# Kernel optimization log

Hardware: AMD Instinct MI355X
Metric: run time of the kernel (lower is better)

The kernel has to match this reference:

```python
import jax, jax.numpy as jnp
import numpy as np

H = 2048   # hidden_size
E = 4096   # intermediate_size
N = 16     # ssm_state_size
K = 4      # conv_kernel
R = 128    # time_step_rank
B_SZ = 2
L = 2048


def setup_inputs() -> dict:
    key = jax.random.key(0)
    ks = jax.random.split(key, 9)
    s = lambda fan: 1.0 / np.sqrt(fan)
    hidden_states = jax.random.normal(ks[0], (B_SZ, L, H), dtype=jnp.float32)
    in_proj_w = jax.random.normal(ks[1], (2 * E, H), dtype=jnp.float32) * s(H)
    conv_w = jax.random.normal(ks[2], (E, 1, K), dtype=jnp.float32) * s(K)
    conv_b = jax.random.normal(ks[3], (E,), dtype=jnp.float32) * 0.01
    x_proj_w = jax.random.normal(ks[4], (R + 2 * N, E), dtype=jnp.float32) * s(E)
    dt_proj_w = jax.random.normal(ks[5], (E, R), dtype=jnp.float32) * s(R)
    dt_proj_b = jax.random.normal(ks[6], (E,), dtype=jnp.float32) * 0.01
    A_log = jnp.log(jnp.broadcast_to(jnp.arange(1, N + 1, dtype=jnp.float32)[None, :], (E, N)))
    D = jnp.ones((E,), dtype=jnp.float32)
    out_proj_w = jax.random.normal(ks[7], (H, E), dtype=jnp.float32) * s(E)
    return {
        "hidden_states": hidden_states,
        "in_proj_w": in_proj_w,
        "conv_w": conv_w,
        "conv_b": conv_b,
        "x_proj_w": x_proj_w,
        "dt_proj_w": dt_proj_w,
        "dt_proj_b": dt_proj_b,
        "A_log": A_log,
        "D": D,
        "out_proj_w": out_proj_w,
    }


def _mamba_fwd(hidden_states, in_proj_w, conv_w, conv_b, x_proj_w,
               dt_proj_w, dt_proj_b, A_log, D, out_proj_w):
    # in_proj -> [B, L, 2E] -> transpose -> [B, 2E, L] -> chunk
    proj = jnp.einsum('blh,eh->ble', hidden_states, in_proj_w)
    proj = jnp.transpose(proj, (0, 2, 1))              # [B, 2E, L]
    u, gate = jnp.split(proj, 2, axis=1)               # each [B, E, L]

    # causal depthwise conv1d (pad K-1 left), then silu
    x = jax.lax.conv_general_dilated(
        u, conv_w, window_strides=(1,), padding=[(K - 1, 0)],
        dimension_numbers=('NCH', 'OIH', 'NCH'), feature_group_count=E)
    x = jax.nn.silu(x + conv_b[None, :, None])          # [B, E, L]

    # x_proj -> dt, B, C
    x_bl = jnp.transpose(x, (0, 2, 1))                  # [B, L, E]
    x_dbl = jnp.einsum('ble,re->blr', x_bl, x_proj_w)   # [B, L, R+2N]
    dt_low, Bmat, Cmat = jnp.split(x_dbl, [R, R + N], axis=-1)
    dt = jax.nn.softplus(jnp.einsum('blr,er->ble', dt_low, dt_proj_w) + dt_proj_b)  # [B, L, E]

    A = -jnp.exp(A_log)                                 # [E, N]

    # selective scan over time; carry state [B, E, N]
    def step(s, inp):
        dt_t, u_t, B_t, C_t = inp                       # [B,E],[B,E],[B,N],[B,N]
        dA = jnp.exp(dt_t[..., None] * A[None])         # [B, E, N]
        s = s * dA + (dt_t * u_t)[..., None] * B_t[:, None, :]
        y_t = jnp.einsum('ben,bn->be', s, C_t)
        return s, y_t

    xs = (jnp.transpose(dt, (1, 0, 2)),                 # [L, B, E]
          jnp.transpose(x, (2, 0, 1)),                  # [L, B, E]
          jnp.transpose(Bmat, (1, 0, 2)),               # [L, B, N]
          jnp.transpose(Cmat, (1, 0, 2)))               # [L, B, N]
    s0 = jnp.zeros((hidden_states.shape[0], E, N), dtype=jnp.float32)
    _, ys = jax.lax.scan(step, s0, xs)                  # ys: [L, B, E]

    y = jnp.transpose(ys, (1, 2, 0))                    # [B, E, L]
    y = y + x * D[None, :, None]
    y = y * jax.nn.silu(gate)
    out = jnp.einsum('bel,he->blh', y, out_proj_w)      # [B, L, H]
    return out


def reference(hidden_states, in_proj_w, conv_w, conv_b, x_proj_w,
              dt_proj_w, dt_proj_b, A_log, D, out_proj_w):
    return _mamba_fwd(hidden_states, in_proj_w, conv_w, conv_b, x_proj_w,
                      dt_proj_w, dt_proj_b, A_log, D, out_proj_w)
```

## Files before the change

kernel.cpp:

```cpp
#include <hip/hip_runtime.h>
#include <math.h>

#define Hd 2048
#define Ed 4096
#define Nssm 16
#define Rrank 128
#define Bb 2
#define Ll 2048
#define Mrows (Bb*Ll)
#define XDBL_C 160
#define Cc 64
#define Tc (Ll/Cc)

typedef unsigned short u16;
typedef short bf16x8 __attribute__((ext_vector_type(8)));
typedef float f32x4 __attribute__((ext_vector_type(4)));
typedef u16 us4 __attribute__((ext_vector_type(4)));
typedef u16 us8 __attribute__((ext_vector_type(8)));

__device__ __forceinline__ u16 f2bf(float f) {
    unsigned u = __float_as_uint(f);
    u += 0x7FFFu + ((u >> 16) & 1u);
    return (u16)(u >> 16);
}
__device__ __forceinline__ float bf2f(u16 h) {
    return __uint_as_float((unsigned)h << 16);
}
__device__ __forceinline__ float fexp(float x)  { return __expf(x); }
__device__ __forceinline__ float fsig(float x)  { return __builtin_amdgcn_rcpf(1.f + __expf(-x)); }
__device__ __forceinline__ float fsoftplus(float z) {
    return fmaxf(z, 0.f) + __logf(1.f + __expf(-fabsf(z)));
}

__device__ __forceinline__ void stage_tile(const char* g, int ldbytes, char* lds, int tid)
{
#pragma unroll
    for (int q = 0; q < 4; ++q) {
        int idx = q * 256 + tid;
        int row = idx >> 3;
        int cb  = (idx & 7) << 4;
        int sb  = cb ^ ((row & 7) << 4);
        __builtin_amdgcn_global_load_lds(
            (const __attribute__((address_space(1))) void*)(g + (size_t)row * ldbytes + sb),
            (__attribute__((address_space(3))) void*)(lds + (size_t)idx * 16),
            16, 0, 0);
    }
}

__device__ __forceinline__ void stage_half(const char* g, int ldbytes, char* lds, int tid)
{
#pragma unroll
    for (int q = 0; q < 2; ++q) {
        int idx = q * 512 + tid;
        int row = idx >> 3;
        int cb  = (idx & 7) << 4;
        int sb  = cb ^ ((row & 7) << 4);
        __builtin_amdgcn_global_load_lds(
            (const __attribute__((address_space(1))) void*)(g + (size_t)row * ldbytes + sb),
            (__attribute__((address_space(3))) void*)(lds + (size_t)idx * 16),
            16, 0, 0);
    }
}

#define NK8  32
#define NKP8 16

__global__ __launch_bounds__(512, 2)
void gemm_8ph_inproj(const u16* __restrict__ A, const u16* __restrict__ Bw,
                     u16* __restrict__ C)
{
    __shared__ __align__(16) char lds[131072];
    const int tid = threadIdx.x;
    const int bm = blockIdx.y * 256;
    const int bn = blockIdx.x * 256;
    const int lane = tid & 63;
    const int wv = tid >> 6;
    const int wm = wv >> 2;
    const int wn = wv & 3;
    const int lr = lane & 15, kg = lane >> 4;

    f32x4 acc[8][4];
#pragma unroll
    for (int m = 0; m < 8; ++m)
#pragma unroll
        for (int n = 0; n < 4; ++n) acc[m][n] = (f32x4){0.f, 0.f, 0.f, 0.f};

    bf16x8 av[8], bv[4];

#define ASLOT(d, h) (lds + ((d)*2 + (h)) * 16384)
#define BSLOT(d, h) (lds + 65536 + ((d)*2 + (h)) * 16384)

#define STAGE_AH(t, h) stage_half((const char*)A  + ((size_t)(bm + (h)*128) * Hd + (t)*64) * 2, Hd*2, ASLOT((t)&1, h), tid)
#define STAGE_BH(t, h) stage_half((const char*)Bw + ((size_t)(bn + (h)*128) * Hd + (t)*64) * 2, Hd*2, BSLOT((t)&1, h), tid)

#define READ_ASUB(d, s) { \
    const char* slot_ = ASLOT(d, wm); \
    _Pragma("unroll") for (int f = 0; f < 4; ++f) { \
        int row = (s)*64 + f*16 + lr; int sw = (row & 7) << 4; \
        const char* rb = slot_ + row * 128; \
        av[f*2+0] = *(const bf16x8*)(rb + ((kg*16) ^ sw)); \
        av[f*2+1] = *(const bf16x8*)(rb + ((64 + kg*16) ^ sw)); } }
#define READ_BSUB(d, u) { \
    const char* slot_ = BSLOT(d, (wn >> 1)); \
    _Pragma("unroll") for (int f = 0; f < 2; ++f) { \
        int row = (wn & 1)*64 + (u)*32 + f*16 + lr; int sw = (row & 7) << 4; \
        const char* rb = slot_ + row * 128; \
        bv[f*2+0] = *(const bf16x8*)(rb + ((kg*16) ^ sw)); \
        bv[f*2+1] = *(const bf16x8*)(rb + ((64 + kg*16) ^ sw)); } }
#define QUAD(s, u) { \
    _Pragma("unroll") for (int f = 0; f < 4; ++f) \
    _Pragma("unroll") for (int g2 = 0; g2 < 2; ++g2) { \
        acc[(s)*4+f][(u)*2+g2] = __builtin_amdgcn_mfma_f32_16x16x32_bf16(av[f*2+0], bv[g2*2+0], acc[(s)*4+f][(u)*2+g2], 0, 0, 0); \
        acc[(s)*4+f][(u)*2+g2] = __builtin_amdgcn_mfma_f32_16x16x32_bf16(av[f*2+1], bv[g2*2+1], acc[(s)*4+f][(u)*2+g2], 0, 0, 0); } }

#define BAR __builtin_amdgcn_s_barrier()
#define PRIO_MFMA(s, u) BAR; __builtin_amdgcn_s_setprio(1); QUAD(s, u); __builtin_amdgcn_s_setprio(0)
#define VMW(n) { asm volatile("s_waitcnt vmcnt(" #n ")" ::: "memory"); __builtin_amdgcn_sched_barrier(0); }

    STAGE_BH(0, 0); STAGE_BH(0, 1); STAGE_AH(0, 0); STAGE_AH(0, 1);
    STAGE_BH(1, 0);
    VMW(2);
    BAR;

    for (int i = 0; i < NKP8; ++i) {
        const int o = 2*i + 1, t2 = 2*i + 2, t3 = 2*i + 3;
        READ_ASUB(0, 0); READ_BSUB(0, 0);
        STAGE_BH(o, 1);
        PRIO_MFMA(0, 0); BAR;
        READ_ASUB(0, 1);
        STAGE_AH(o, 0);
        PRIO_MFMA(1, 0); BAR;
        READ_BSUB(0, 1);
        STAGE_AH(o, 1);
        PRIO_MFMA(1, 1); BAR;
        READ_ASUB(0, 0);
        if (t2 < NK8) STAGE_BH(t2, 0);
        PRIO_MFMA(0, 1);
        if (i == NKP8 - 1) { VMW(0); } else { VMW(2); }
        BAR;
        READ_ASUB(1, 0); READ_BSUB(1, 0);
        if (t2 < NK8) STAGE_BH(t2, 1);
        PRIO_MFMA(0, 0); BAR;
        READ_ASUB(1, 1);
        if (t2 < NK8) STAGE_AH(t2, 0);
        PRIO_MFMA(1, 0); BAR;
        READ_BSUB(1, 1);
        if (t2 < NK8) STAGE_AH(t2, 1);
        PRIO_MFMA(1, 1); BAR;
        READ_ASUB(1, 0);
        if (t3 < NK8) STAGE_BH(t3, 0);
        PRIO_MFMA(0, 1);
        VMW(2);
        BAR;
    }

#pragma unroll
    for (int m = 0; m < 8; ++m) {
        int rbase = bm + wm * 128 + m * 16 + kg * 4;
#pragma unroll
        for (int n = 0; n < 4; ++n) {
            int col = bn + wn * 64 + n * 16 + lr;
#pragma unroll
            for (int r = 0; r < 4; ++r)
                C[(size_t)(rbase + r) * (2 * Ed) + col] = f2bf(acc[m][n][r]);
        }
    }
#undef ASLOT
#undef BSLOT
#undef STAGE_AH
#undef STAGE_BH
#undef READ_ASUB
#undef READ_BSUB
#undef QUAD
#undef BAR
#undef PRIO_MFMA
#undef VMW
}

template<int EPI, int CBF16>
__global__ __launch_bounds__(256)
void gemm_bf16(const u16* __restrict__ A, const u16* __restrict__ Bw,
               void* __restrict__ Cp, const float* __restrict__ bias,
               int Nv, int Ksub, int lda, int ldb, int ldc, size_t zstride)
{
    __shared__ __align__(16) char lds[32768];
    char* ldsA = lds;
    char* ldsB = lds + 16384;
    const int tid = threadIdx.x;
    const int bm = blockIdx.y * 128;
    const int bn = blockIdx.x * 128;
    const int lane = tid & 63, wv = tid >> 6;
    const int wr = (wv >> 1) * 64, wc = (wv & 1) * 64;
    const int lr = lane & 15, kg = lane >> 4;
    const int kbeg = blockIdx.z * Ksub;

    f32x4 acc[4][4];
#pragma unroll
    for (int m = 0; m < 4; ++m)
#pragma unroll
        for (int n = 0; n < 4; ++n) acc[m][n] = (f32x4){0.f, 0.f, 0.f, 0.f};

    for (int k0 = kbeg; k0 < kbeg + Ksub; k0 += 64) {
        stage_tile((const char*)A  + ((size_t)bm * lda + k0) * 2, lda * 2, ldsA, tid);
        stage_tile((const char*)Bw + ((size_t)bn * ldb + k0) * 2, ldb * 2, ldsB, tid);
        __syncthreads();
#pragma unroll
        for (int kk = 0; kk < 2; ++kk) {
            const int bc = kk * 64 + kg * 16;
            bf16x8 bfr[4], af[4];
#pragma unroll
            for (int n = 0; n < 4; ++n) {
                int row = wc + n * 16 + lr;
                bfr[n] = *(const bf16x8*)(ldsB + row * 128 + (bc ^ ((row & 7) << 4)));
            }
#pragma unroll
            for (int m = 0; m < 4; ++m) {
                int row = wr + m * 16 + lr;
                af[m] = *(const bf16x8*)(ldsA + row * 128 + (bc ^ ((row & 7) << 4)));
            }
#pragma unroll
            for (int m = 0; m < 4; ++m)
#pragma unroll
                for (int n = 0; n < 4; ++n)
                    acc[m][n] = __builtin_amdgcn_mfma_f32_16x16x32_bf16(af[m], bfr[n], acc[m][n], 0, 0, 0);
        }
        __syncthreads();
    }

    if (zstride) Cp = (void*)((float*)Cp + (size_t)blockIdx.z * zstride);

#pragma unroll
    for (int m = 0; m < 4; ++m) {
        int rbase = bm + wr + m * 16 + kg * 4;
#pragma unroll
        for (int n = 0; n < 4; ++n) {
            int col = bn + wc + n * 16 + lr;
            if (col < Nv) {
#pragma unroll
                for (int r = 0; r < 4; ++r) {
                    float v = acc[m][n][r];
                    if (EPI == 1) v = fsoftplus(v + bias[col]);
                    if (CBF16) ((u16*)Cp)[(size_t)(rbase + r) * ldc + col] = f2bf(v);
                    else       ((float*)Cp)[(size_t)(rbase + r) * ldc + col] = v;
                }
            }
        }
    }
}

__global__ __launch_bounds__(256)
void reduce_cast(const float* __restrict__ part, float* __restrict__ outf,
                 u16* __restrict__ outb, int cnt, size_t stride, int total)
{
    int i = blockIdx.x * 256 + threadIdx.x;
    if (i < total) {
        float v = 0.f;
        for (int z = 0; z < cnt; z++) v += part[(size_t)z * stride + i];
        outf[i] = v;
        outb[i] = f2bf(v);
    }
}

__global__ __launch_bounds__(256)
void cast_w(const float* __restrict__ s, u16* __restrict__ d, int n)
{
    int i = (blockIdx.x * 256 + threadIdx.x) * 8;
    if (i >= n) return;
    float4 a = *(const float4*)(s + i);
    float4 b = *(const float4*)(s + i + 4);
    us8 o;
    o[0] = f2bf(a.x); o[1] = f2bf(a.y); o[2] = f2bf(a.z); o[3] = f2bf(a.w);
    o[4] = f2bf(b.x); o[5] = f2bf(b.y); o[6] = f2bf(b.z); o[7] = f2bf(b.w);
    *(us8*)(d + i) = o;
}

__global__ __launch_bounds__(256)
void cast_wx(const float* __restrict__ s, u16* __restrict__ d)
{
    int i4 = (blockIdx.x * 256 + threadIdx.x) * 4;
    int row = i4 >> 12;
    us4 o = (us4){0, 0, 0, 0};
    if (row < XDBL_C) {
        float4 v = *(const float4*)(s + i4);
        o[0] = f2bf(v.x); o[1] = f2bf(v.y); o[2] = f2bf(v.z); o[3] = f2bf(v.w);
    }
    *(us4*)(d + i4) = o;
}

__global__ __launch_bounds__(256)
void conv_silu_bf(const u16* __restrict__ proj, const float* __restrict__ cw,
                  const float* __restrict__ cb, u16* __restrict__ x)
{
    const int e  = blockIdx.x * 256 + threadIdx.x;
    const int t0 = blockIdx.y * 32;
    const int bz = blockIdx.z;
    const float4 w4 = *(const float4*)(cw + (size_t)e * 4);
    const float bias = cb[e];
    const size_t base = (size_t)bz * Ll * (2 * Ed) + e;

    float u0 = 0.f, u1 = 0.f, u2 = 0.f;
    if (t0 >= 3) {
        u0 = bf2f(proj[base + (size_t)(t0 - 3) * (2 * Ed)]);
        u1 = bf2f(proj[base + (size_t)(t0 - 2) * (2 * Ed)]);
        u2 = bf2f(proj[base + (size_t)(t0 - 1) * (2 * Ed)]);
    }
    size_t xo = ((size_t)(bz * Ll + t0)) * Ed + e;
#pragma unroll 4
    for (int t = t0; t < t0 + 32; ++t) {
        float u3 = bf2f(proj[base + (size_t)t * (2 * Ed)]);
        float acc = bias;
        acc = fmaf(w4.x, u0, acc);
        acc = fmaf(w4.y, u1, acc);
        acc = fmaf(w4.z, u2, acc);
        acc = fmaf(w4.w, u3, acc);
        float sx = acc * fsig(acc);
        x[xo] = f2bf(sx);
        xo += Ed;
        u0 = u1; u1 = u2; u2 = u3;
    }
}

__global__ __launch_bounds__(256)
void scan_part1(const u16* __restrict__ proj, const u16* __restrict__ x,
                const float* __restrict__ xdbl, const float* __restrict__ Alog,
                float* __restrict__ S, float* __restrict__ sumdt)
{
    const int e = blockIdx.x * 256 + threadIdx.x;
    const int c = blockIdx.y;
    const int b = blockIdx.z;

    float Ae[Nssm];
#pragma unroll
    for (int n = 0; n < Nssm; n++) Ae[n] = -fexp(Alog[(size_t)e * Nssm + n]);

    float s[Nssm];
#pragma unroll
    for (int n = 0; n < Nssm; n++) s[n] = 0.f;
    float sdt = 0.f;

    const size_t row0 = (size_t)b * Ll + (size_t)c * Tc;
    for (int t = 0; t < Tc; ++t) {
        size_t r = row0 + t;
        float dtv = bf2f(proj[r * (2 * Ed) + e]);
        float uv  = bf2f(x[r * Ed + e]);
        const float* p = xdbl + r * XDBL_C + Rrank;
        float du = dtv * uv;
        sdt += dtv;
#pragma unroll
        for (int n = 0; n < Nssm; n++)
            s[n] = fmaf(s[n], fexp(dtv * Ae[n]), du * p[n]);
    }

    float* sp = S + ((((size_t)b * Cc + c) * Ed + e) * Nssm);
#pragma unroll
    for (int n = 0; n < Nssm; n += 4)
        *(float4*)(sp + n) = make_float4(s[n], s[n+1], s[n+2], s[n+3]);
    sumdt[((size_t)b * Cc + c) * Ed + e] = sdt;
}

__global__ __launch_bounds__(256)
void scan_mid(float* __restrict__ S, const float* __restrict__ sumdt,
              const float* __restrict__ Alog)
{
    const int idx = blockIdx.x * 256 + threadIdx.x;
    const int n = idx & (Nssm - 1);
    const int e = (idx >> 4) & (Ed - 1);
    const int b = idx >> 16;
    const float Ae = -fexp(Alog[(size_t)e * Nssm + n]);
    float carry = 0.f;
    for (int c = 0; c < Cc; ++c) {
        size_t off = (((size_t)b * Cc + c) * Ed + e) * Nssm + n;
        float sl = S[off];
        float P  = fexp(Ae * sumdt[((size_t)b * Cc + c) * Ed + e]);
        S[off] = carry;
        carry = fmaf(P, carry, sl);
    }
}

__global__ __launch_bounds__(256)
void scan_part2(const u16* __restrict__ proj, u16* __restrict__ x,
                const float* __restrict__ xdbl, const float* __restrict__ Alog,
                const float* __restrict__ Dvec, const float* __restrict__ S)
{
    const int e = blockIdx.x * 256 + threadIdx.x;
    const int c = blockIdx.y;
    const int b = blockIdx.z;

    float Ae[Nssm];
#pragma unroll
    for (int n = 0; n < Nssm; n++) Ae[n] = -fexp(Alog[(size_t)e * Nssm + n]);
    const float Dv = Dvec[e];

    float s[Nssm];
    const float* sp = S + ((((size_t)b * Cc + c) * Ed + e) * Nssm);
#pragma unroll
    for (int n = 0; n < Nssm; n += 4) {
        float4 v = *(const float4*)(sp + n);
        s[n] = v.x; s[n+1] = v.y; s[n+2] = v.z; s[n+3] = v.w;
    }

    const size_t row0 = (size_t)b * Ll + (size_t)c * Tc;
    for (int t = 0; t < Tc; ++t) {
        size_t r = row0 + t;
        float dtv = bf2f(proj[r * (2 * Ed) + e]);
        float uv  = bf2f(x[r * Ed + e]);
        float gv  = bf2f(proj[r * (2 * Ed) + Ed + e]);
        const float* p = xdbl + r * XDBL_C + Rrank;
        float du = dtv * uv;
        float y = 0.f;
#pragma unroll
        for (int n = 0; n < Nssm; n++) {
            float dA = fexp(dtv * Ae[n]);
            s[n] = fmaf(s[n], dA, du * p[n]);
            y = fmaf(s[n], p[Nssm + n], y);
        }
        float yv = (y + uv * Dv) * (gv * fsig(gv));
        x[r * Ed + e] = f2bf(yv);
    }
}

extern "C" void kernel_launch(void* const* d_in, const int* in_sizes, int n_in,
                              void* d_out, int out_size, void* d_ws, size_t ws_size,
                              hipStream_t stream) {
    const float* hs    = (const float*)d_in[0];
    const float* w_in  = (const float*)d_in[1];
    const float* cw    = (const float*)d_in[2];
    const float* cb    = (const float*)d_in[3];
    const float* w_x   = (const float*)d_in[4];
    const float* w_dt  = (const float*)d_in[5];
    const float* b_dt  = (const float*)d_in[6];
    const float* Alog  = (const float*)d_in[7];
    const float* Dvec  = (const float*)d_in[8];
    const float* w_out = (const float*)d_in[9];
    float* out = (float*)d_out;

    char* w = (char*)d_ws;
    u16*  proj_bf  = (u16*)w;
    u16*  x_bf     = (u16*)(w + 67108864);
    u16*  w_in_bf  = (u16*)(w + 100663296);
    u16*  w_out_bf = (u16*)(w + 134217728);
    u16*  hs_bf    = (u16*)(w + 150994944);
    u16*  w_x_bf   = (u16*)(w + 167772160);
    u16*  w_dt_bf  = (u16*)(w + 169869312);
    float* xdbl    = (float*)(w + 170917888);
    u16*  xdbl_bf  = (u16*)(w + 173539328);
    float* part    = (float*)(w + 174850048);
    float* sumdt   = (float*)(w + 185335808);
    float* S       = (float*)(w + 187432960);

    dim3 blk(256);

    cast_w<<<dim3(8192), blk, 0, stream>>>(w_in, w_in_bf, 2 * Ed * Hd);
    cast_w<<<dim3(4096), blk, 0, stream>>>(w_out, w_out_bf, Hd * Ed);
    cast_w<<<dim3(256),  blk, 0, stream>>>(w_dt, w_dt_bf, Ed * Rrank);
    cast_wx<<<dim3(1024), blk, 0, stream>>>(w_x, w_x_bf);
    cast_w<<<dim3(4096), blk, 0, stream>>>(hs, hs_bf, Mrows * Hd);

    gemm_8ph_inproj<<<dim3(2 * Ed / 256, Mrows / 256), dim3(512), 0, stream>>>(
        hs_bf, w_in_bf, proj_bf);

    conv_silu_bf<<<dim3(Ed / 256, Ll / 32, Bb), blk, 0, stream>>>(proj_bf, cw, cb, x_bf);

    gemm_bf16<0, 0><<<dim3(2, 32, 4), blk, 0, stream>>>(
        x_bf, w_x_bf, part, nullptr, XDBL_C, Ed / 4, Ed, Ed, XDBL_C,
        (size_t)Mrows * XDBL_C);
    reduce_cast<<<dim3((Mrows * XDBL_C + 255) / 256), blk, 0, stream>>>(
        part, xdbl, xdbl_bf, 4, (size_t)Mrows * XDBL_C, Mrows * XDBL_C);

    gemm_bf16<1, 1><<<dim3(32, 32, 1), blk, 0, stream>>>(
        xdbl_bf, w_dt_bf, proj_bf, b_dt, Ed, Rrank, XDBL_C, Rrank, 2 * Ed, 0);

    scan_part1<<<dim3(Ed / 256, Cc, Bb), blk, 0, stream>>>(
        proj_bf, x_bf, xdbl, Alog, S, sumdt);
    scan_mid<<<dim3(Bb * Ed * Nssm / 256), blk, 0, stream>>>(S, sumdt, Alog);
    scan_part2<<<dim3(Ed / 256, Cc, Bb), blk, 0, stream>>>(
        proj_bf, x_bf, xdbl, Alog, Dvec, S);

    gemm_bf16<0, 0><<<dim3(16, 32, 1), blk, 0, stream>>>(
        x_bf, w_out_bf, out, nullptr, Hd, Ed, Ed, Ed, Hd, 0);
}
```

Baseline: 437.4 us.

## Replace in/out projection GEMMs with shared triple-buffered 256x128 kernel

Introduces a templated triple-buffered LDS GEMM with a 256x128 tile and uses it for both the in_proj and out_proj GEMMs. It replaces the double-buffered 256x256 in_proj kernel and the generic 128x128 gemm for out_proj. The deeper prefetch is meant to hide global load latency and the smaller N tile to increase block count. The 144KB LDS footprint likely limits residency to one block per CU, and smaller tiles reduce operand reuse.

```diff
diff --git a/kernel.cpp b/kernel.cpp
--- a/kernel.cpp
+++ b/kernel.cpp
@@ -62,118 +62,97 @@
     }
 }
 
-#define NK8  32
-#define NKP8 16
-
+template<int NKT, int CBF16>
 __global__ __launch_bounds__(512, 2)
-void gemm_8ph_inproj(const u16* __restrict__ A, const u16* __restrict__ Bw,
-                     u16* __restrict__ C)
-{
-    __shared__ __align__(16) char lds[131072];
+void gemm_3buf(const u16* __restrict__ A, const u16* __restrict__ Bw,
+               void* __restrict__ Cp, int ld, int ldc)
+{
+    __shared__ __align__(16) char lds[147456];
     const int tid = threadIdx.x;
     const int bm = blockIdx.y * 256;
-    const int bn = blockIdx.x * 256;
+    const int bn = blockIdx.x * 128;
     const int lane = tid & 63;
     const int wv = tid >> 6;
-    const int wm = wv >> 2;
-    const int wn = wv & 3;
+    const int wm = wv >> 1;
+    const int wn = wv & 1;
     const int lr = lane & 15, kg = lane >> 4;
 
-    f32x4 acc[8][4];
-#pragma unroll
-    for (int m = 0; m < 8; ++m)
-#pragma unroll
-        for (int n = 0; n < 4; ++n) acc[m][n] = (f32x4){0.f, 0.f, 0.f, 0.f};
-
-    bf16x8 av[8], bv[4];
-
-#define ASLOT(d, h) (lds + ((d)*2 + (h)) * 16384)
-#define BSLOT(d, h) (lds + 65536 + ((d)*2 + (h)) * 16384)
-
-#define STAGE_AH(t, h) stage_half((const char*)A  + ((size_t)(bm + (h)*128) * Hd + (t)*64) * 2, Hd*2, ASLOT((t)&1, h), tid)
-#define STAGE_BH(t, h) stage_half((const char*)Bw + ((size_t)(bn + (h)*128) * Hd + (t)*64) * 2, Hd*2, BSLOT((t)&1, h), tid)
-
-#define READ_ASUB(d, s) { \
-    const char* slot_ = ASLOT(d, wm); \
+    f32x4 acc[4][4];
+#pragma unroll
+    for (int f = 0; f < 4; ++f)
+#pragma unroll
+        for (int g = 0; g < 4; ++g) acc[f][g] = (f32x4){0.f, 0.f, 0.f, 0.f};
+
+    bf16x8 av[4][2], bv[2][2];
+
+#define BUFA(b) (lds + (b) * 49152)
+#define BUFB(b) (lds + (b) * 49152 + 32768)
+#define STAGE_A3(t, b) { \
+    stage_half((const char*)A + ((size_t)(bm)       * ld + (t)*64) * 2, ld*2, BUFA(b), tid); \
+    stage_half((const char*)A + ((size_t)(bm + 128) * ld + (t)*64) * 2, ld*2, BUFA(b) + 16384, tid); }
+#define STAGE_B3(t, b) \
+    stage_half((const char*)Bw + ((size_t)(bn)      * ld + (t)*64) * 2, ld*2, BUFB(b), tid)
+#define READ_A3(b) { const char* p_ = BUFA(b); \
     _Pragma("unroll") for (int f = 0; f < 4; ++f) { \
-        int row = (s)*64 + f*16 + lr; int sw = (row & 7) << 4; \
-        const char* rb = slot_ + row * 128; \
-        av[f*2+0] = *(const bf16x8*)(rb + ((kg*16) ^ sw)); \
-        av[f*2+1] = *(const bf16x8*)(rb + ((64 + kg*16) ^ sw)); } }
-#define READ_BSUB(d, u) { \
-    const char* slot_ = BSLOT(d, (wn >> 1)); \
-    _Pragma("unroll") for (int f = 0; f < 2; ++f) { \
-        int row = (wn & 1)*64 + (u)*32 + f*16 + lr; int sw = (row & 7) << 4; \
-        const char* rb = slot_ + row * 128; \
-        bv[f*2+0] = *(const bf16x8*)(rb + ((kg*16) ^ sw)); \
-        bv[f*2+1] = *(const bf16x8*)(rb + ((64 + kg*16) ^ sw)); } }
-#define QUAD(s, u) { \
+        int row = wm*64 + f*16 + lr; int sw = (row & 7) << 4; \
+        const char* rb = p_ + row * 128; \
+        av[f][0] = *(const bf16x8*)(rb + ((kg*16) ^ sw)); \
+        av[f][1] = *(const bf16x8*)(rb + ((64 + kg*16) ^ sw)); } }
+#define READ_B3(b, u) { const char* p_ = BUFB(b); \
+    _Pragma("unroll") for (int g = 0; g < 2; ++g) { \
+        int row = wn*64 + (u)*32 + g*16 + lr; int sw = (row & 7) << 4; \
+        const char* rb = p_ + row * 128; \
+        bv[g][0] = *(const bf16x8*)(rb + ((kg*16) ^ sw)); \
+        bv[g][1] = *(const bf16x8*)(rb + ((64 + kg*16) ^ sw)); } }
+#define QUAD3(u) { \
     _Pragma("unroll") for (int f = 0; f < 4; ++f) \
-    _Pragma("unroll") for (int g2 = 0; g2 < 2; ++g2) { \
-        acc[(s)*4+f][(u)*2+g2] = __builtin_amdgcn_mfma_f32_16x16x32_bf16(av[f*2+0], bv[g2*2+0], acc[(s)*4+f][(u)*2+g2], 0, 0, 0); \
-        acc[(s)*4+f][(u)*2+g2] = __builtin_amdgcn_mfma_f32_16x16x32_bf16(av[f*2+1], bv[g2*2+1], acc[(s)*4+f][(u)*2+g2], 0, 0, 0); } }
-
+    _Pragma("unroll") for (int g = 0; g < 2; ++g) { \
+        acc[f][(u)*2+g] = __builtin_amdgcn_mfma_f32_16x16x32_bf16(av[f][0], bv[g][0], acc[f][(u)*2+g], 0, 0, 0); \
+        acc[f][(u)*2+g] = __builtin_amdgcn_mfma_f32_16x16x32_bf16(av[f][1], bv[g][1], acc[f][(u)*2+g], 0, 0, 0); } }
 #define BAR __builtin_amdgcn_s_barrier()
-#define PRIO_MFMA(s, u) BAR; __builtin_amdgcn_s_setprio(1); QUAD(s, u); __builtin_amdgcn_s_setprio(0)
 #define VMW(n) { asm volatile("s_waitcnt vmcnt(" #n ")" ::: "memory"); __builtin_amdgcn_sched_barrier(0); }
 
-    STAGE_BH(0, 0); STAGE_BH(0, 1); STAGE_AH(0, 0); STAGE_AH(0, 1);
-    STAGE_BH(1, 0);
-    VMW(2);
+    STAGE_A3(0, 0); STAGE_B3(0, 0);
+    STAGE_A3(1, 1); STAGE_B3(1, 1);
+    VMW(6);
     BAR;
 
-    for (int i = 0; i < NKP8; ++i) {
-        const int o = 2*i + 1, t2 = 2*i + 2, t3 = 2*i + 3;
-        READ_ASUB(0, 0); READ_BSUB(0, 0);
-        STAGE_BH(o, 1);
-        PRIO_MFMA(0, 0); BAR;
-        READ_ASUB(0, 1);
-        STAGE_AH(o, 0);
-        PRIO_MFMA(1, 0); BAR;
-        READ_BSUB(0, 1);
-        STAGE_AH(o, 1);
-        PRIO_MFMA(1, 1); BAR;
-        READ_ASUB(0, 0);
-        if (t2 < NK8) STAGE_BH(t2, 0);
-        PRIO_MFMA(0, 1);
-        if (i == NKP8 - 1) { VMW(0); } else { VMW(2); }
+    int bc = 0;
+    for (int t = 0; t < NKT; ++t) {
+        int b2 = bc + 2; if (b2 >= 3) b2 -= 3;
+        READ_A3(bc); READ_B3(bc, 0);
+        if (t + 2 < NKT) STAGE_A3(t + 2, b2);
+        BAR; __builtin_amdgcn_s_setprio(1); QUAD3(0); __builtin_amdgcn_s_setprio(0); BAR;
+        READ_B3(bc, 1);
+        if (t + 2 < NKT) STAGE_B3(t + 2, b2);
+        BAR; __builtin_amdgcn_s_setprio(1); QUAD3(1); __builtin_amdgcn_s_setprio(0);
+        if (t + 2 < NKT) { VMW(6); } else if (t + 1 < NKT) { VMW(0); }
         BAR;
-        READ_ASUB(1, 0); READ_BSUB(1, 0);
-        if (t2 < NK8) STAGE_BH(t2, 1);
-        PRIO_MFMA(0, 0); BAR;
-        READ_ASUB(1, 1);
-        if (t2 < NK8) STAGE_AH(t2, 0);
-        PRIO_MFMA(1, 0); BAR;
-        READ_BSUB(1, 1);
-        if (t2 < NK8) STAGE_AH(t2, 1);
-        PRIO_MFMA(1, 1); BAR;
-        READ_ASUB(1, 0);
-        if (t3 < NK8) STAGE_BH(t3, 0);
-        PRIO_MFMA(0, 1);
-        VMW(2);
-        BAR;
-    }
-
-#pragma unroll
-    for (int m = 0; m < 8; ++m) {
-        int rbase = bm + wm * 128 + m * 16 + kg * 4;
-#pragma unroll
-        for (int n = 0; n < 4; ++n) {
-            int col = bn + wn * 64 + n * 16 + lr;
-#pragma unroll
-            for (int r = 0; r < 4; ++r)
-                C[(size_t)(rbase + r) * (2 * Ed) + col] = f2bf(acc[m][n][r]);
+        bc = (bc + 1 == 3) ? 0 : bc + 1;
+    }
+
+#pragma unroll
+    for (int f = 0; f < 4; ++f) {
+        int rbase = bm + wm * 64 + f * 16 + kg * 4;
+#pragma unroll
+        for (int g = 0; g < 4; ++g) {
+            int col = bn + wn * 64 + g * 16 + lr;
+#pragma unroll
+            for (int r = 0; r < 4; ++r) {
+                float v = acc[f][g][r];
+                if (CBF16) ((u16*)Cp)[(size_t)(rbase + r) * ldc + col] = f2bf(v);
+                else       ((float*)Cp)[(size_t)(rbase + r) * ldc + col] = v;
+            }
         }
     }
-#undef ASLOT
-#undef BSLOT
-#undef STAGE_AH
-#undef STAGE_BH
-#undef READ_ASUB
-#undef READ_BSUB
-#undef QUAD
+#undef BUFA
+#undef BUFB
+#undef STAGE_A3
+#undef STAGE_B3
+#undef READ_A3
+#undef READ_B3
+#undef QUAD3
 #undef BAR
-#undef PRIO_MFMA
 #undef VMW
 }
 
@@ -456,8 +435,8 @@
     cast_wx<<<dim3(1024), blk, 0, stream>>>(w_x, w_x_bf);
     cast_w<<<dim3(4096), blk, 0, stream>>>(hs, hs_bf, Mrows * Hd);
 
-    gemm_8ph_inproj<<<dim3(2 * Ed / 256, Mrows / 256), dim3(512), 0, stream>>>(
-        hs_bf, w_in_bf, proj_bf);
+    gemm_3buf<Hd / 64, 1><<<dim3(2 * Ed / 128, Mrows / 256), dim3(512), 0, stream>>>(
+        hs_bf, w_in_bf, proj_bf, Hd, 2 * Ed);
 
     conv_silu_bf<<<dim3(Ed / 256, Ll / 32, Bb), blk, 0, stream>>>(proj_bf, cw, cb, x_bf);
 
@@ -476,6 +455,6 @@
     scan_part2<<<dim3(Ed / 256, Cc, Bb), blk, 0, stream>>>(
         proj_bf, x_bf, xdbl, Alog, Dvec, S);
 
-    gemm_bf16<0, 0><<<dim3(16, 32, 1), blk, 0, stream>>>(
-        x_bf, w_out_bf, out, nullptr, Hd, Ed, Ed, Ed, Hd, 0);
-}
+    gemm_3buf<Ed / 64, 0><<<dim3(Hd / 128, Mrows / 256), dim3(512), 0, stream>>>(
+        x_bf, w_out_bf, out, Ed, Hd);
+}
```

Measured after the change: 418.9 us. -4.2%, faster.
